# Kernel optimization log

Measured on AMD Instinct MI355X. Metric: run time of the kernel, lower is better.

Reference implementation:

```python
import jax, jax.numpy as jnp
import numpy as np
import math

BATCH, SEQ, D_CONTENT = 16, 512, 1024
D_POSITION, NUM_TILES, D_HIDDEN = 64, 8, 4096


def _make_pe(max_len, d_model):
    pe = np.zeros((max_len, d_model), dtype=np.float32)
    position = np.arange(max_len, dtype=np.float32)[:, None]
    div_term = np.exp(np.arange(0, d_model, 2, dtype=np.float32) * (-math.log(10000.0) / d_model))
    pe[:, 0::2] = np.sin(position * div_term)
    pe[:, 1::2] = np.cos(position * div_term)
    return jnp.asarray(pe)


def setup_inputs() -> dict:
    key = jax.random.key(0)
    ks = jax.random.split(key, 8)
    x = jax.random.normal(ks[0], (BATCH, SEQ, D_CONTENT), dtype=jnp.float32)
    pe = _make_pe(SEQ, D_POSITION)  # (SEQ, D_POSITION), buffer sliced to seq len
    position_weight = jnp.asarray(0.5, dtype=jnp.float32)
    content_weight = jnp.asarray(0.5, dtype=jnp.float32)
    pos_sigs = jax.random.normal(ks[1], (NUM_TILES, D_POSITION), dtype=jnp.float32)
    content_sigs = jax.random.normal(ks[2], (NUM_TILES, D_CONTENT), dtype=jnp.float32)
    s1 = 1.0 / math.sqrt(D_CONTENT)
    s2 = 1.0 / math.sqrt(D_HIDDEN)
    W1 = jax.random.normal(ks[3], (NUM_TILES, D_CONTENT, D_HIDDEN), dtype=jnp.float32) * s1
    b1 = jax.random.normal(ks[4], (NUM_TILES, D_HIDDEN), dtype=jnp.float32) * s1
    W2 = jax.random.normal(ks[5], (NUM_TILES, D_HIDDEN, D_CONTENT), dtype=jnp.float32) * s2
    b2 = jax.random.normal(ks[6], (NUM_TILES, D_CONTENT), dtype=jnp.float32) * s2
    return {"x": x, "pe": pe, "position_weight": position_weight,
            "content_weight": content_weight, "pos_sigs": pos_sigs,
            "content_sigs": content_sigs, "W1": W1, "b1": b1, "W2": W2, "b2": b2}


def reference(x, pe, position_weight, content_weight, pos_sigs, content_sigs, W1, b1, W2, b2):
    B, S, _ = x.shape
    num_tiles = W1.shape[0]
    # normalized position/content mixing weights
    pw = jax.nn.sigmoid(position_weight)
    cw = jax.nn.sigmoid(content_weight)
    tot = pw + cw
    pw, cw = pw / tot, cw / tot
    # mixed address: [pw * pos_enc | cw * x] -> (B, S, Dp + Dc)
    pos_part = jnp.broadcast_to((pw * pe[:S])[None], (B, S, pe.shape[-1]))
    address = jnp.concatenate([pos_part, cw * x], axis=-1)
    # ternarized signatures (T, Dp + Dc)
    signatures = jnp.concatenate([jnp.sign(pos_sigs), jnp.sign(content_sigs)], axis=-1)
    scores = jnp.einsum('bsd,td->bst', address, signatures)
    indices = jnp.argmax(scores, axis=-1)  # (B, S) top-1 tile per token
    # dispatch: per-tile gelu MLP, combined via top-1 mask (loop over fixed small tile count)
    out = jnp.zeros_like(x)
    for t in range(num_tiles):
        h = jax.nn.gelu(jnp.einsum('bsd,dh->bsh', x, W1[t]) + b1[t], approximate=False)
        y = jnp.einsum('bsh,hd->bsd', h, W2[t]) + b2[t]
        out = out + jnp.where((indices == t)[..., None], y, jnp.zeros((), x.dtype))
    return out
```

## Files before the change

kernel.cpp:

```cpp
#include <hip/hip_runtime.h>
#include <hip/hip_bf16.h>
#include <math.h>

#define BATCH 16
#define SEQ   512
#define DC    1024
#define DP    64
#define NT    8
#define DH    4096
#define NTOK  (BATCH*SEQ)

#define BM 128
#define BN 128
#define BK 32

typedef __attribute__((ext_vector_type(8))) short short8;
typedef __attribute__((ext_vector_type(4))) float floatx4;
typedef __attribute__((ext_vector_type(4))) unsigned short ushort4v;
typedef __attribute__((ext_vector_type(8))) unsigned short ushort8v;

__device__ __forceinline__ unsigned short f2bf(float f) {
  union { float f; unsigned u; } v; v.f = f;
  unsigned r = v.u + 0x7FFFu + ((v.u >> 16) & 1u);
  return (unsigned short)(r >> 16);
}

__device__ __forceinline__ void gl_lds16(const void* g, void* l) {
  __builtin_amdgcn_global_load_lds(
      (__attribute__((address_space(1))) void*)g,
      (__attribute__((address_space(3))) void*)l, 16, 0, 0);
}

__global__ __launch_bounds__(256) void route_kernel(
    const float* __restrict__ x, const float* __restrict__ pe,
    const float* __restrict__ pwp, const float* __restrict__ cwp,
    const float* __restrict__ pos_sigs, const float* __restrict__ csigs,
    int* __restrict__ counts, int* __restrict__ list,
    unsigned short* __restrict__ xb) {
  int wid  = threadIdx.x >> 6;
  int lane = threadIdx.x & 63;
  int token = blockIdx.x * 4 + wid;
  int s = token & (SEQ - 1);

  float pwr = 1.f / (1.f + expf(-pwp[0]));
  float cwr = 1.f / (1.f + expf(-cwp[0]));
  float tot = pwr + cwr;
  float pw = pwr / tot, cw = cwr / tot;

  float acc[NT];
#pragma unroll
  for (int t = 0; t < NT; t++) acc[t] = 0.f;

  float a0 = pw * pe[s * DP + lane];
#pragma unroll
  for (int t = 0; t < NT; t++) {
    float v = pos_sigs[t * DP + lane];
    float sg = (v > 0.f) ? 1.f : ((v < 0.f) ? -1.f : 0.f);
    acc[t] = fmaf(a0, sg, acc[t]);
  }

  const float* xrow = x + (size_t)token * DC;
  unsigned short* xbrow = xb + (size_t)token * DC;
#pragma unroll 4
  for (int i = 0; i < DC / 64; i++) {
    int c = lane + i * 64;
    float xv = xrow[c];
    xbrow[c] = f2bf(xv);
    float a = cw * xv;
#pragma unroll
    for (int t = 0; t < NT; t++) {
      float v = csigs[t * DC + c];
      float sg = (v > 0.f) ? 1.f : ((v < 0.f) ? -1.f : 0.f);
      acc[t] = fmaf(a, sg, acc[t]);
    }
  }

#pragma unroll
  for (int off = 32; off >= 1; off >>= 1)
#pragma unroll
    for (int t = 0; t < NT; t++) acc[t] += __shfl_xor(acc[t], off);

  if (lane == 0) {
    int best = 0; float bv = acc[0];
#pragma unroll
    for (int t = 1; t < NT; t++)
      if (acc[t] > bv) { bv = acc[t]; best = t; }
    int slot = atomicAdd(&counts[best], 1);
    list[best * NTOK + slot] = token;
  }
}

template<int AR, int AC>
__global__ __launch_bounds__(256) void transpose_kernel(
    const float* __restrict__ in, unsigned short* __restrict__ out) {
  __shared__ unsigned short tile[64 * 65];
  int t = blockIdx.z;
  const float* in_t = in + (size_t)t * AR * AC;
  unsigned short* out_t = out + (size_t)t * AR * AC;
  int x0 = blockIdx.x * 64, y0 = blockIdx.y * 64;
  int tid = threadIdx.x;
  int ry = tid >> 2, cx = (tid & 3) * 16;
  const float* src = in_t + (size_t)(y0 + ry) * AC + x0 + cx;
  float4 v0 = *(const float4*)(src);
  float4 v1 = *(const float4*)(src + 4);
  float4 v2 = *(const float4*)(src + 8);
  float4 v3 = *(const float4*)(src + 12);
  unsigned short* trow = &tile[ry * 65 + cx];
  trow[0]  = f2bf(v0.x); trow[1]  = f2bf(v0.y); trow[2]  = f2bf(v0.z); trow[3]  = f2bf(v0.w);
  trow[4]  = f2bf(v1.x); trow[5]  = f2bf(v1.y); trow[6]  = f2bf(v1.z); trow[7]  = f2bf(v1.w);
  trow[8]  = f2bf(v2.x); trow[9]  = f2bf(v2.y); trow[10] = f2bf(v2.z); trow[11] = f2bf(v2.w);
  trow[12] = f2bf(v3.x); trow[13] = f2bf(v3.y); trow[14] = f2bf(v3.z); trow[15] = f2bf(v3.w);
  __syncthreads();
  int rx = tid >> 2, cy = (tid & 3) * 16;
  ushort8v o0, o1;
#pragma unroll
  for (int j = 0; j < 8; j++) o0[j] = tile[(cy + j) * 65 + rx];
#pragma unroll
  for (int j = 0; j < 8; j++) o1[j] = tile[(cy + 8 + j) * 65 + rx];
  size_t ob = (size_t)(x0 + rx) * AR + y0 + cy;
  *(ushort8v*)&out_t[ob]     = o0;
  *(ushort8v*)&out_t[ob + 8] = o1;
}

template<int K, int N, int NXB, bool GELU>
__global__ __launch_bounds__(256) void gemm_pipe_kernel(
    const unsigned short* __restrict__ A, const unsigned short* __restrict__ BT,
    const float* __restrict__ bias, const int* __restrict__ counts,
    const int* __restrict__ list, unsigned short* __restrict__ Hout,
    float* __restrict__ Fout) {
  unsigned bid = blockIdx.x;
  int t = bid & (NT - 1);
  unsigned inner = bid >> 3;
  int bx = inner & (NXB - 1);
  int by = inner / NXB;

  int count = counts[t];
  int base = by * BM;
  if (base >= count) return;
  int j0 = bx * BN;

  __shared__ __align__(16) unsigned short As[3][BM * BK];
  __shared__ __align__(16) unsigned short Bs[3][BN * BK];
  __shared__ int toks[BM];

  int tid = threadIdx.x;
  if (tid < BM) {
    int slot = base + tid;
    toks[tid] = (slot < count) ? list[t * NTOK + slot] : -1;
  }
  __syncthreads();

  int w = tid >> 6, lane = tid & 63;
  int lrow = lane >> 2;
  int lc   = lane & 3;
  int swz  = (lc ^ ((lrow >> 1) & 3)) * 8;

  const unsigned short* srcA[2];
  const unsigned short* srcB[2];
  int cho[2];
#pragma unroll
  for (int i = 0; i < 2; i++) {
    int ch = i * 4 + w;
    int r = ch * 16 + lrow;
    int tk = toks[r]; if (tk < 0) tk = 0;
    srcA[i] = A + (size_t)tk * K + swz;
    srcB[i] = BT + (size_t)t * N * K + (size_t)(j0 + r) * K + swz;
    cho[i] = ch * 512;
  }

  int wm = (w & 1) * 64, wn = (w >> 1) * 64;
  int quad = lane >> 4, l15 = lane & 15;
  int fswz = (quad ^ ((l15 >> 1) & 3)) * 8;

  floatx4 acc[4][4];
#pragma unroll
  for (int mi = 0; mi < 4; mi++)
#pragma unroll
    for (int ni = 0; ni < 4; ni++) acc[mi][ni] = (floatx4){0.f, 0.f, 0.f, 0.f};

  constexpr int S = K / BK;
  unsigned short *a0 = As[0], *a1 = As[1], *a2 = As[2];
  unsigned short *b0 = Bs[0], *b1 = Bs[1], *b2 = Bs[2];

#pragma unroll
  for (int i = 0; i < 2; i++) {
    gl_lds16(srcA[i], a0 + cho[i]); gl_lds16(srcB[i], b0 + cho[i]);
    srcA[i] += BK; srcB[i] += BK;
  }
#pragma unroll
  for (int i = 0; i < 2; i++) {
    gl_lds16(srcA[i], a1 + cho[i]); gl_lds16(srcB[i], b1 + cho[i]);
    srcA[i] += BK; srcB[i] += BK;
  }
  asm volatile("s_waitcnt vmcnt(4)" ::: "memory");
  __builtin_amdgcn_s_barrier();

#pragma unroll 1
  for (int k = 0; k < S - 1; ++k) {
    short8 a[4], b[4];
#pragma unroll
    for (int mi = 0; mi < 4; mi++)
      a[mi] = *(const short8*)&a0[(wm + mi * 16 + l15) * BK + fswz];
#pragma unroll
    for (int ni = 0; ni < 4; ni++)
      b[ni] = *(const short8*)&b0[(wn + ni * 16 + l15) * BK + fswz];

    if (k < S - 2) {
#pragma unroll
      for (int i = 0; i < 2; i++) {
        gl_lds16(srcA[i], a2 + cho[i]); gl_lds16(srcB[i], b2 + cho[i]);
        srcA[i] += BK; srcB[i] += BK;
      }
    }

    __builtin_amdgcn_s_setprio(1);
#pragma unroll
    for (int mi = 0; mi < 4; mi++)
#pragma unroll
      for (int ni = 0; ni < 4; ni++)
        acc[mi][ni] = __builtin_amdgcn_mfma_f32_16x16x32_bf16(a[mi], b[ni], acc[mi][ni], 0, 0, 0);
    __builtin_amdgcn_s_setprio(0);

    if (k < S - 2) {
      asm volatile("s_waitcnt vmcnt(4)" ::: "memory");
    } else {
      asm volatile("s_waitcnt vmcnt(0)" ::: "memory");
    }
    __builtin_amdgcn_s_barrier();

    unsigned short* tp;
    tp = a0; a0 = a1; a1 = a2; a2 = tp;
    tp = b0; b0 = b1; b1 = b2; b2 = tp;
  }

  {
    short8 a[4], b[4];
#pragma unroll
    for (int mi = 0; mi < 4; mi++)
      a[mi] = *(const short8*)&a0[(wm + mi * 16 + l15) * BK + fswz];
#pragma unroll
    for (int ni = 0; ni < 4; ni++)
      b[ni] = *(const short8*)&b0[(wn + ni * 16 + l15) * BK + fswz];
#pragma unroll
    for (int mi = 0; mi < 4; mi++)
#pragma unroll
      for (int ni = 0; ni < 4; ni++)
        acc[mi][ni] = __builtin_amdgcn_mfma_f32_16x16x32_bf16(a[mi], b[ni], acc[mi][ni], 0, 0, 0);
  }

#pragma unroll
  for (int ni = 0; ni < 4; ni++) {
    int n = j0 + wn + ni * 16 + l15;
    float bv = bias[t * N + n];
#pragma unroll
    for (int mi = 0; mi < 4; mi++) {
      int mb = wm + mi * 16 + quad * 4;
#pragma unroll
      for (int r = 0; r < 4; r++) {
        int tok = toks[mb + r];
        if (tok >= 0) {
          float v = acc[mi][ni][r] + bv;
          if (GELU) {
            v = 0.5f * v * (1.f + erff(v * 0.70710678118654752f));
            Hout[(size_t)tok * N + n] = f2bf(v);
          } else {
            Fout[(size_t)tok * N + n] = v;
          }
        }
      }
    }
  }
}

#define KPAD 40
__global__ __launch_bounds__(256) void gemm1_fb(
    const unsigned short* __restrict__ xb, const float* __restrict__ W1,
    const float* __restrict__ b1, const int* __restrict__ counts,
    const int* __restrict__ list, unsigned short* __restrict__ H) {
  int t = blockIdx.z;
  int count = counts[t];
  int base = blockIdx.y * BM;
  if (base >= count) return;
  int j0 = blockIdx.x * BN;
  __shared__ unsigned short As[BM][KPAD];
  __shared__ unsigned short Bs[BN][KPAD];
  __shared__ int toks[BM];
  int tid = threadIdx.x;
  if (tid < BM) {
    int slot = base + tid;
    toks[tid] = (slot < count) ? list[t * NTOK + slot] : -1;
  }
  __syncthreads();
  int arow = tid >> 1, acol = (tid & 1) * 16;
  int mytok = toks[arow];
  const unsigned short* xrow = xb + (size_t)(mytok < 0 ? 0 : mytok) * DC;
  int kg4 = (tid >> 5) * 4, ng4 = (tid & 31) * 4;
  const float* Wt = W1 + (size_t)t * DC * DH;
  int wid = tid >> 6, lane = tid & 63;
  int wm = (wid & 1) * 64, wn = (wid >> 1) * 64;
  int quad = lane >> 4, l15 = lane & 15;
  floatx4 acc[4][4];
#pragma unroll
  for (int mi = 0; mi < 4; mi++)
#pragma unroll
    for (int ni = 0; ni < 4; ni++) acc[mi][ni] = (floatx4){0.f, 0.f, 0.f, 0.f};
  for (int kt = 0; kt < DC / BK; kt++) {
    int k0 = kt * BK;
    if (mytok >= 0) {
      *(uint4*)&As[arow][acol]     = *(const uint4*)(xrow + k0 + acol);
      *(uint4*)&As[arow][acol + 8] = *(const uint4*)(xrow + k0 + acol + 8);
    } else {
      uint4 z = {0u,0u,0u,0u};
      *(uint4*)&As[arow][acol] = z; *(uint4*)&As[arow][acol + 8] = z;
    }
    const float* wb = Wt + (size_t)(k0 + kg4) * DH + j0 + ng4;
    float4 r0 = *(const float4*)(wb);
    float4 r1 = *(const float4*)(wb + DH);
    float4 r2 = *(const float4*)(wb + 2 * DH);
    float4 r3 = *(const float4*)(wb + 3 * DH);
    ushort4v c0 = { f2bf(r0.x), f2bf(r1.x), f2bf(r2.x), f2bf(r3.x) };
    ushort4v c1 = { f2bf(r0.y), f2bf(r1.y), f2bf(r2.y), f2bf(r3.y) };
    ushort4v c2 = { f2bf(r0.z), f2bf(r1.z), f2bf(r2.z), f2bf(r3.z) };
    ushort4v c3 = { f2bf(r0.w), f2bf(r1.w), f2bf(r2.w), f2bf(r3.w) };
    *(ushort4v*)&Bs[ng4 + 0][kg4] = c0; *(ushort4v*)&Bs[ng4 + 1][kg4] = c1;
    *(ushort4v*)&Bs[ng4 + 2][kg4] = c2; *(ushort4v*)&Bs[ng4 + 3][kg4] = c3;
    __syncthreads();
    short8 a[4], b[4];
#pragma unroll
    for (int mi = 0; mi < 4; mi++) a[mi] = *(const short8*)&As[wm + mi * 16 + l15][quad * 8];
#pragma unroll
    for (int ni = 0; ni < 4; ni++) b[ni] = *(const short8*)&Bs[wn + ni * 16 + l15][quad * 8];
#pragma unroll
    for (int mi = 0; mi < 4; mi++)
#pragma unroll
      for (int ni = 0; ni < 4; ni++)
        acc[mi][ni] = __builtin_amdgcn_mfma_f32_16x16x32_bf16(a[mi], b[ni], acc[mi][ni], 0, 0, 0);
    __syncthreads();
  }
#pragma unroll
  for (int ni = 0; ni < 4; ni++) {
    int n = j0 + wn + ni * 16 + l15;
    float bias = b1[t * DH + n];
#pragma unroll
    for (int mi = 0; mi < 4; mi++) {
      int mb = wm + mi * 16 + quad * 4;
#pragma unroll
      for (int r = 0; r < 4; r++) {
        int tok = toks[mb + r];
        if (tok >= 0) {
          float v = acc[mi][ni][r] + bias;
          v = 0.5f * v * (1.f + erff(v * 0.70710678118654752f));
          H[(size_t)tok * DH + n] = f2bf(v);
        }
      }
    }
  }
}

__global__ __launch_bounds__(256) void gemm2_fb(
    const unsigned short* __restrict__ H, const float* __restrict__ W2,
    const float* __restrict__ b2, const int* __restrict__ counts,
    const int* __restrict__ list, float* __restrict__ out) {
  int t = blockIdx.z;
  int count = counts[t];
  int base = blockIdx.y * BM;
  if (base >= count) return;
  int j0 = blockIdx.x * BN;
  __shared__ unsigned short As[BM][KPAD];
  __shared__ unsigned short Bs[BN][KPAD];
  __shared__ int toks[BM];
  int tid = threadIdx.x;
  if (tid < BM) {
    int slot = base + tid;
    toks[tid] = (slot < count) ? list[t * NTOK + slot] : -1;
  }
  __syncthreads();
  int arow = tid >> 1, acol = (tid & 1) * 16;
  int mytok = toks[arow];
  const unsigned short* hrow = H + (size_t)(mytok < 0 ? 0 : mytok) * DH;
  int kg4 = (tid >> 5) * 4, ng4 = (tid & 31) * 4;
  const float* Wt = W2 + (size_t)t * DH * DC;
  int wid = tid >> 6, lane = tid & 63;
  int wm = (wid & 1) * 64, wn = (wid >> 1) * 64;
  int quad = lane >> 4, l15 = lane & 15;
  floatx4 acc[4][4];
#pragma unroll
  for (int mi = 0; mi < 4; mi++)
#pragma unroll
    for (int ni = 0; ni < 4; ni++) acc[mi][ni] = (floatx4){0.f, 0.f, 0.f, 0.f};
  for (int kt = 0; kt < DH / BK; kt++) {
    int k0 = kt * BK;
    if (mytok >= 0) {
      *(uint4*)&As[arow][acol]     = *(const uint4*)(hrow + k0 + acol);
      *(uint4*)&As[arow][acol + 8] = *(const uint4*)(hrow + k0 + acol + 8);
    } else {
      uint4 z = {0u,0u,0u,0u};
      *(uint4*)&As[arow][acol] = z; *(uint4*)&As[arow][acol + 8] = z;
    }
    const float* wb = Wt + (size_t)(k0 + kg4) * DC + j0 + ng4;
    float4 r0 = *(const float4*)(wb);
    float4 r1 = *(const float4*)(wb + DC);
    float4 r2 = *(const float4*)(wb + 2 * DC);
    float4 r3 = *(const float4*)(wb + 3 * DC);
    ushort4v c0 = { f2bf(r0.x), f2bf(r1.x), f2bf(r2.x), f2bf(r3.x) };
    ushort4v c1 = { f2bf(r0.y), f2bf(r1.y), f2bf(r2.y), f2bf(r3.y) };
    ushort4v c2 = { f2bf(r0.z), f2bf(r1.z), f2bf(r2.z), f2bf(r3.z) };
    ushort4v c3 = { f2bf(r0.w), f2bf(r1.w), f2bf(r2.w), f2bf(r3.w) };
    *(ushort4v*)&Bs[ng4 + 0][kg4] = c0; *(ushort4v*)&Bs[ng4 + 1][kg4] = c1;
    *(ushort4v*)&Bs[ng4 + 2][kg4] = c2; *(ushort4v*)&Bs[ng4 + 3][kg4] = c3;
    __syncthreads();
    short8 a[4], b[4];
#pragma unroll
    for (int mi = 0; mi < 4; mi++) a[mi] = *(const short8*)&As[wm + mi * 16 + l15][quad * 8];
#pragma unroll
    for (int ni = 0; ni < 4; ni++) b[ni] = *(const short8*)&Bs[wn + ni * 16 + l15][quad * 8];
#pragma unroll
    for (int mi = 0; mi < 4; mi++)
#pragma unroll
      for (int ni = 0; ni < 4; ni++)
        acc[mi][ni] = __builtin_amdgcn_mfma_f32_16x16x32_bf16(a[mi], b[ni], acc[mi][ni], 0, 0, 0);
    __syncthreads();
  }
#pragma unroll
  for (int ni = 0; ni < 4; ni++) {
    int n = j0 + wn + ni * 16 + l15;
    float bias = b2[t * DC + n];
#pragma unroll
    for (int mi = 0; mi < 4; mi++) {
      int mb = wm + mi * 16 + quad * 4;
#pragma unroll
      for (int r = 0; r < 4; r++) {
        int tok = toks[mb + r];
        if (tok >= 0) out[(size_t)tok * DC + n] = acc[mi][ni][r] + bias;
      }
    }
  }
}

extern "C" void kernel_launch(void* const* d_in, const int* in_sizes, int n_in,
                              void* d_out, int out_size, void* d_ws, size_t ws_size,
                              hipStream_t stream) {
  const float* x        = (const float*)d_in[0];
  const float* pe       = (const float*)d_in[1];
  const float* pwp      = (const float*)d_in[2];
  const float* cwp      = (const float*)d_in[3];
  const float* pos_sigs = (const float*)d_in[4];
  const float* csigs    = (const float*)d_in[5];
  const float* W1       = (const float*)d_in[6];
  const float* b1       = (const float*)d_in[7];
  const float* W2       = (const float*)d_in[8];
  const float* b2       = (const float*)d_in[9];
  float* out = (float*)d_out;

  char* ws = (char*)d_ws;
  int* counts = (int*)ws;
  int* list   = (int*)(ws + 1024);
  unsigned short* xb = (unsigned short*)(ws + (1 << 20));

  hipMemsetAsync(counts, 0, NT * sizeof(int), stream);
  route_kernel<<<NTOK / 4, 256, 0, stream>>>(x, pe, pwp, cwp, pos_sigs, csigs,
                                             counts, list, xb);

  if (ws_size >= (size_t)145 * 1024 * 1024) {
    unsigned short* WT = (unsigned short*)(ws + ((size_t)17 << 20));
    unsigned short* H  = (unsigned short*)(ws + ((size_t)81 << 20));

    transpose_kernel<DC, DH><<<dim3(DH / 64, DC / 64, NT), 256, 0, stream>>>(W1, WT);
    gemm_pipe_kernel<DC, DH, DH / BN, true>
        <<<(DH / BN) * (NTOK / BM) * NT, 256, 0, stream>>>(
        xb, WT, b1, counts, list, H, nullptr);
    transpose_kernel<DH, DC><<<dim3(DC / 64, DH / 64, NT), 256, 0, stream>>>(W2, WT);
    gemm_pipe_kernel<DH, DC, DC / BN, false>
        <<<(DC / BN) * (NTOK / BM) * NT, 256, 0, stream>>>(
        H, WT, b2, counts, list, nullptr, out);
  } else {
    unsigned short* H = (unsigned short*)(ws + ((size_t)32 << 20));
    gemm1_fb<<<dim3(DH / BN, NTOK / BM, NT), 256, 0, stream>>>(xb, W1, b1, counts, list, H);
    gemm2_fb<<<dim3(DC / BN, NTOK / BM, NT), 256, 0, stream>>>(H, W2, b2, counts, list, out);
  }
}
```

Measured before the change: 698.7 us.

## Use 256x256-tile, 8-wave ping-pong GEMM kernel for first MoE layer

Adds a new grouped GEMM kernel with 256x256 output tiles, BK=64, 512 threads and double-buffered LDS filled by direct global-to-LDS loads with XOR swizzling. MFMA phases are interleaved with the prefetch of the next K-tile and raised with s_setprio. Only the first (GELU) GEMM uses it. The larger tiles increase reuse per load, but they waste more work on partially filled routed tiles, use much more LDS (about 128KB), and add barriers inside the loop.

```diff
diff --git a/kernel.cpp b/kernel.cpp
--- a/kernel.cpp
+++ b/kernel.cpp
@@ -122,6 +122,147 @@
   *(ushort8v*)&out_t[ob + 8] = o1;
 }
 
+template<int K, int N, bool GELU>
+__global__ __launch_bounds__(512) void gemm8p_kernel(
+    const unsigned short* __restrict__ A, const unsigned short* __restrict__ BT,
+    const float* __restrict__ bias, const int* __restrict__ counts,
+    const int* __restrict__ list, unsigned short* __restrict__ Hout,
+    float* __restrict__ Fout) {
+  int t = blockIdx.z;
+  int count = counts[t];
+  int base = blockIdx.y * 256;
+  if (base >= count) return;
+  int j0 = blockIdx.x * 256;
+
+  __shared__ __align__(16) unsigned short As[2][256 * 64];
+  __shared__ __align__(16) unsigned short Bs[2][256 * 64];
+  __shared__ int toks[256];
+
+  int tid = threadIdx.x;
+  if (tid < 256) {
+    int slot = base + tid;
+    toks[tid] = (slot < count) ? list[t * NTOK + slot] : -1;
+  }
+  __syncthreads();
+
+  int srow = tid >> 3;
+  int sw = (((tid & 7) ^ (srow & 7)) << 3);
+  const unsigned short* gsrcA[4];
+  const unsigned short* gsrcB[4];
+#pragma unroll
+  for (int i = 0; i < 4; i++) {
+    int ra = i * 64 + srow;
+    int tk = toks[ra]; if (tk < 0) tk = 0;
+    gsrcA[i] = A + (size_t)tk * K + sw;
+    gsrcB[i] = BT + ((size_t)t * N + (size_t)(j0 + ra)) * K + sw;
+  }
+  int ldst = tid * 8;
+
+  int w = tid >> 6;
+  int wr = w >> 2, wc = w & 3;
+  int lane = tid & 63;
+  int quad = lane >> 4, l15 = lane & 15;
+  int axor = l15 & 7;
+  int abase = (wr * 128 + l15) * 64;
+  int bbase = (wc * 64 + l15) * 64;
+  int koff0 = ((0 * 4 + quad) ^ axor) << 3;
+  int koff1 = ((1 * 4 + quad) ^ axor) << 3;
+
+  floatx4 acc[8][4];
+#pragma unroll
+  for (int m = 0; m < 8; m++)
+#pragma unroll
+    for (int ni = 0; ni < 4; ni++) acc[m][ni] = (floatx4){0.f, 0.f, 0.f, 0.f};
+
+  constexpr int NKT = K / 64;
+
+#pragma unroll
+  for (int i = 0; i < 4; i++) {
+    gl_lds16(gsrcA[i], &As[0][i * 4096 + ldst]);
+    gl_lds16(gsrcB[i], &Bs[0][i * 4096 + ldst]);
+    gsrcA[i] += 64; gsrcB[i] += 64;
+  }
+  asm volatile("s_waitcnt vmcnt(0)" ::: "memory");
+  __builtin_amdgcn_s_barrier();
+
+#pragma unroll 1
+  for (int kt = 0; kt < NKT; ++kt) {
+    const unsigned short* Ab = As[kt & 1];
+    const unsigned short* Bb = Bs[kt & 1];
+    unsigned short* An = (unsigned short*)As[(kt & 1) ^ 1];
+    unsigned short* Bn = (unsigned short*)Bs[(kt & 1) ^ 1];
+    bool pf = (kt + 1 < NKT);
+
+    short8 bfrag[4];
+#pragma unroll
+    for (int p = 0; p < 4; ++p) {
+      const int kk = p >> 1, ah = p & 1;
+      const int koff = kk ? koff1 : koff0;
+      short8 afrag[4];
+      if (ah == 0) {
+#pragma unroll
+        for (int ni = 0; ni < 4; ni++)
+          bfrag[ni] = *(const short8*)&Bb[bbase + ni * 1024 + koff];
+      }
+#pragma unroll
+      for (int m = 0; m < 4; m++)
+        afrag[m] = *(const short8*)&Ab[abase + (ah * 4 + m) * 1024 + koff];
+
+      if (pf) {
+        if (p < 2) {
+          gl_lds16(gsrcA[2 * p],     An + (2 * p) * 4096 + ldst);
+          gl_lds16(gsrcA[2 * p + 1], An + (2 * p + 1) * 4096 + ldst);
+          gsrcA[2 * p] += 64; gsrcA[2 * p + 1] += 64;
+        } else {
+          const int q = 2 * (p - 2);
+          gl_lds16(gsrcB[q],     Bn + q * 4096 + ldst);
+          gl_lds16(gsrcB[q + 1], Bn + (q + 1) * 4096 + ldst);
+          gsrcB[q] += 64; gsrcB[q + 1] += 64;
+        }
+      }
+
+      __builtin_amdgcn_s_barrier();
+      asm volatile("s_waitcnt lgkmcnt(0)" ::: "memory");
+      __builtin_amdgcn_sched_barrier(0);
+      __builtin_amdgcn_s_setprio(1);
+#pragma unroll
+      for (int ni = 0; ni < 4; ni++)
+#pragma unroll
+        for (int m = 0; m < 4; m++)
+          acc[ah * 4 + m][ni] = __builtin_amdgcn_mfma_f32_16x16x32_bf16(
+              afrag[m], bfrag[ni], acc[ah * 4 + m][ni], 0, 0, 0);
+      __builtin_amdgcn_s_setprio(0);
+      __builtin_amdgcn_sched_barrier(0);
+      if (p == 3 && pf)
+        asm volatile("s_waitcnt vmcnt(0)" ::: "memory");
+      __builtin_amdgcn_s_barrier();
+    }
+  }
+
+#pragma unroll
+  for (int ni = 0; ni < 4; ni++) {
+    int n = j0 + wc * 64 + ni * 16 + l15;
+    float bv = bias[t * N + n];
+#pragma unroll
+    for (int m = 0; m < 8; m++) {
+      int mb = wr * 128 + m * 16 + quad * 4;
+#pragma unroll
+      for (int r = 0; r < 4; r++) {
+        int tok = toks[mb + r];
+        if (tok >= 0) {
+          float v = acc[m][ni][r] + bv;
+          if (GELU) {
+            v = 0.5f * v * (1.f + erff(v * 0.70710678118654752f));
+            Hout[(size_t)tok * N + n] = f2bf(v);
+          } else {
+            Fout[(size_t)tok * N + n] = v;
+          }
+        }
+      }
+    }
+  }
+}
+
 template<int K, int N, int NXB, bool GELU>
 __global__ __launch_bounds__(256) void gemm_pipe_kernel(
     const unsigned short* __restrict__ A, const unsigned short* __restrict__ BT,
@@ -466,8 +607,7 @@
     unsigned short* H  = (unsigned short*)(ws + ((size_t)81 << 20));
 
     transpose_kernel<DC, DH><<<dim3(DH / 64, DC / 64, NT), 256, 0, stream>>>(W1, WT);
-    gemm_pipe_kernel<DC, DH, DH / BN, true>
-        <<<(DH / BN) * (NTOK / BM) * NT, 256, 0, stream>>>(
+    gemm8p_kernel<DC, DH, true><<<dim3(DH / 256, NTOK / 256, NT), 512, 0, stream>>>(
         xb, WT, b1, counts, list, H, nullptr);
     transpose_kernel<DH, DC><<<dim3(DC / 64, DH / 64, NT), 256, 0, stream>>>(W2, WT);
     gemm_pipe_kernel<DH, DC, DC / BN, false>
```

Result: slower. 731.4 us (+4.7%).
